# Kernel optimization log

Hardware: AMD Instinct MI355X
Metric: run time of the kernel (lower is better)

The kernel has to match this reference:

```python
import jax, jax.numpy as jnp
import numpy as np

DIM_Q, DIM_K, DIM_V, H = 256, 256, 384, 6
B, N = 8, 1024
NEG = -10.0 ** 10  # matches torch's (1 - A) * -10**10


def sparsemax(z):
    # simplex projection along last axis (Martins & Astudillo 2016)
    z = z - jnp.max(z, axis=-1, keepdims=True)  # shift-invariant, for fp stability
    z_sorted = jnp.flip(jnp.sort(z, axis=-1), axis=-1)          # descending
    k = jnp.arange(1, z.shape[-1] + 1, dtype=z.dtype)
    z_cumsum = jnp.cumsum(z_sorted, axis=-1)
    support = (1.0 + k * z_sorted) > z_cumsum
    k_z = jnp.sum(support, axis=-1, keepdims=True)              # int32 support size >= 1
    tau = (jnp.take_along_axis(z_cumsum, k_z - 1, axis=-1) - 1.0) / k_z.astype(z.dtype)
    return jnp.maximum(z - tau, 0.0)


def setup_inputs() -> dict:
    key = jax.random.key(0)
    ks = jax.random.split(key, 7)
    Q = jax.random.normal(ks[0], (B, N, DIM_Q), jnp.float32)
    V = jax.random.normal(ks[1], (B, N, DIM_K), jnp.float32)
    # binary adjacency mask with self-loops so every row has support
    A = jax.random.bernoulli(ks[2], 0.05, (B, N, N)).astype(jnp.float32)
    A = A.at[:, jnp.arange(N), jnp.arange(N)].set(1.0)
    # torch.nn.Linear default init: U(-1/sqrt(fan_in), 1/sqrt(fan_in)); weights stored pre-transposed [in, out]
    sq = 1.0 / np.sqrt(DIM_Q)
    sk = 1.0 / np.sqrt(DIM_K)
    WQ = jax.random.uniform(ks[3], (DIM_Q, DIM_V), jnp.float32, -sq, sq)
    bQ = jax.random.uniform(ks[4], (DIM_V,), jnp.float32, -sq, sq)
    WK = jax.random.uniform(ks[5], (DIM_K, DIM_V), jnp.float32, -sk, sk)
    bK = jax.random.uniform(ks[6], (DIM_V,), jnp.float32, -sk, sk)
    return {"Q": Q, "V": V, "A": A, "WQ": WQ, "bQ": bQ, "WK": WK, "bK": bK}


def reference(Q, V, A, WQ, bQ, WK, bK):
    b, n, _ = Q.shape
    d = DIM_V // H
    # project and split heads (torch split along dim=2 == reshape [b,n,H,d])
    q = (Q @ WQ + bQ).reshape(b, n, H, d).transpose(0, 2, 1, 3)   # [b,H,n,d]
    k = (V @ WK + bK).reshape(b, n, H, d).transpose(0, 2, 1, 3)   # [b,H,n,d]
    scale = 1.0 / jnp.sqrt(jnp.float32(DIM_V))
    logits = jnp.einsum('bhnd,bhmd->bhnm', q, k) * scale + (1.0 - A)[:, None] * NEG
    O = sparsemax(logits)                                          # [b,H,n,n], rows on simplex
    # torch: split(B) along dim0 then cat along dim2 -> head-major along last axis
    return O.transpose(0, 2, 1, 3).reshape(b, n, H * n)            # [b,n,H*n]
```

## Files before the change

kernel.cpp:

```cpp
#include <hip/hip_runtime.h>
#include <hip/hip_bf16.h>
#include <stdint.h>

#define DIMK 256
#define DIMV 384
#define NSEQ 1024
#define NHEAD 6
#define ZCAP 192

typedef __attribute__((ext_vector_type(8))) short short8;
typedef __attribute__((ext_vector_type(4))) float floatx4;

__device__ __forceinline__ unsigned short f2b(float f){
  unsigned int x = __float_as_uint(f);
  return (unsigned short)((x + 0x7fffu + ((x >> 16) & 1u)) >> 16);
}
__device__ __forceinline__ unsigned int pack2(float a, float b){
  return (unsigned int)f2b(a) | ((unsigned int)f2b(b) << 16);
}
__device__ __forceinline__ float blo(unsigned int u){ return __uint_as_float(u << 16); }

__global__ __launch_bounds__(256) void prep_kernel(
    const float* __restrict__ WQ, const float* __restrict__ WK,
    unsigned short* __restrict__ wqt, unsigned short* __restrict__ wkt,
    const float* __restrict__ A,
    unsigned long long* __restrict__ bm, unsigned short* __restrict__ bmp)
{
  int bid = blockIdx.x;
  if (bid < 768){
    int i = bid * 256 + threadIdx.x;
    const float* W; unsigned short* O; int idx;
    if (i < 98304){ W = WQ; O = wqt; idx = i; }
    else          { W = WK; O = wkt; idx = i - 98304; }
    int n = idx >> 8;
    int k = idx & 255;
    O[idx] = f2b(W[(size_t)k * 384 + n]);
  } else {
    int r = (bid - 768) * 4 + (threadIdx.x >> 6);
    int lane = threadIdx.x & 63;
    const float* arow = A + (size_t)r * NSEQ;
    unsigned long long myw = 0;
    #pragma unroll
    for (int c = 0; c < 16; ++c){
      unsigned long long m = __ballot(arow[c * 64 + lane] > 0.5f);
      if (lane == c) myw = m;
    }
    int own = (lane < 16) ? __popcll(myw) : 0;
    int inc = own;
    #pragma unroll
    for (int o = 1; o < 16; o <<= 1){
      int t = __shfl_up(inc, o, 16);
      if ((lane & 15) >= o) inc += t;
    }
    if (lane < 16){
      bm [(size_t)r * 16 + lane] = myw;
      bmp[(size_t)r * 16 + lane] = (unsigned short)(inc - own);
    }
  }
}

__global__ __launch_bounds__(256) void proj2_kernel(
    const float* __restrict__ Q, const float* __restrict__ V,
    const unsigned short* __restrict__ wqt, const unsigned short* __restrict__ wkt,
    const float* __restrict__ bQ, const float* __restrict__ bK,
    unsigned short* __restrict__ qhi, unsigned short* __restrict__ qlo,
    unsigned short* __restrict__ kf)
{
  __shared__ uint4 lA[512];
  __shared__ uint4 lB[864];
  int which = blockIdx.z;
  const float* X = which ? V : Q;
  const unsigned short* Wt = which ? wkt : wqt;
  const float* bias = which ? bK : bQ;

  int t = threadIdx.x;
  int lane = t & 63, wave = t >> 6;
  int wm = wave >> 1, wn = wave & 1;
  int rb = blockIdx.x * 64;
  int nb = blockIdx.y * 96;
  floatx4 acc[2][3];
  #pragma unroll
  for (int mi = 0; mi < 2; ++mi)
    #pragma unroll
    for (int ni = 0; ni < 3; ++ni) acc[mi][ni] = (floatx4){0.f, 0.f, 0.f, 0.f};

  for (int it = 0; it < 4; ++it){
    int k0 = it * 64;
    #pragma unroll
    for (int i = 0; i < 2; ++i){
      int c = t + i * 256;
      int kc = c >> 6, row = c & 63;
      const float* src = X + (size_t)(rb + row) * DIMK + k0 + kc * 8;
      float4 f0 = *(const float4*)src;
      float4 f1 = *(const float4*)(src + 4);
      uint4 w;
      w.x = pack2(f0.x, f0.y); w.y = pack2(f0.z, f0.w);
      w.z = pack2(f1.x, f1.y); w.w = pack2(f1.z, f1.w);
      lA[c] = w;
    }
    #pragma unroll
    for (int i = 0; i < 3; ++i){
      int c = t + i * 256;
      int n = c >> 3, kc = c & 7;
      uint4 v = *(const uint4*)(Wt + (size_t)(nb + n) * DIMK + k0 + kc * 8);
      lB[n * 9 + kc] = v;
    }
    __syncthreads();
    #pragma unroll
    for (int kk = 0; kk < 2; ++kk){
      int kc  = kk * 4 + (lane >> 4);
      int r16 = lane & 15;
      short8 af[2], bf[3];
      #pragma unroll
      for (int mi = 0; mi < 2; ++mi)
        af[mi] = *(const short8*)&lA[kc * 64 + wm * 32 + mi * 16 + r16];
      #pragma unroll
      for (int ni = 0; ni < 3; ++ni)
        bf[ni] = *(const short8*)&lB[(wn * 48 + ni * 16 + r16) * 9 + kc];
      #pragma unroll
      for (int mi = 0; mi < 2; ++mi)
        #pragma unroll
        for (int ni = 0; ni < 3; ++ni)
          acc[mi][ni] = __builtin_amdgcn_mfma_f32_16x16x32_bf16(af[mi], bf[ni], acc[mi][ni], 0, 0, 0);
    }
    __syncthreads();
  }
  const float scale = 0.05103103630798288f;
  int r16 = lane & 15, rq = lane >> 4;
  #pragma unroll
  for (int ni = 0; ni < 3; ++ni){
    int col = nb + wn * 48 + ni * 16 + r16;
    float bv = bias[col];
    int h = col >> 6, d = col & 63;
    #pragma unroll
    for (int mi = 0; mi < 2; ++mi){
      #pragma unroll
      for (int q = 0; q < 4; ++q){
        int row = rb + wm * 32 + mi * 16 + rq * 4 + q;
        int bb = row >> 10, n = row & 1023;
        int slice = bb * NHEAD + h;
        size_t dst = ((((size_t)slice * 2 + (d >> 5)) * 64 + (n >> 4)) * 64
                      + ((d >> 3) & 3) * 16 + (n & 15)) * 8 + (d & 7);
        float v = acc[mi][ni][q] + bv;
        if (which){
          kf[dst] = f2b(v);
        } else {
          v *= scale;
          unsigned short hi_ = f2b(v);
          qhi[dst] = hi_;
          qlo[dst] = f2b(v - blo((unsigned int)hi_));
        }
      }
    }
  }
}

__device__ __forceinline__ void red2(float& a, float& b){
  #pragma unroll
  for (int o = 1; o < 64; o <<= 1){ a += __shfl_xor(a, o); b += __shfl_xor(b, o); }
}
__device__ __forceinline__ void red4(float& a, float& b, float& c, float& d){
  #pragma unroll
  for (int o = 1; o < 64; o <<= 1){
    a += __shfl_xor(a, o); b += __shfl_xor(b, o);
    c += __shfl_xor(c, o); d += __shfl_xor(d, o);
  }
}

__global__ __launch_bounds__(512) void attn_kernel(
    const unsigned short* __restrict__ qhi, const unsigned short* __restrict__ qlo,
    const unsigned short* __restrict__ kf, const unsigned long long* __restrict__ bm,
    const unsigned short* __restrict__ bmp, float* __restrict__ out)
{
  __shared__ unsigned long long mw[16][16];
  __shared__ unsigned short    mp[16][16];
  __shared__ float             zlds[16][ZCAP + 1];

  int bid = blockIdx.x;
  int x = bid & 7;
  int u = bid >> 3;
  int h = u >> 6;
  int rb = u & 63;
  int tid = threadIdx.x;
  int lane = tid & 63, w = tid >> 6;
  int slice = x * NHEAD + h;
  int rowbase = (x << 10) + (rb << 4);

  if (tid < 256){
    int rr = tid >> 4, ww = tid & 15;
    mw[rr][ww] = bm [((size_t)(rowbase + rr)) * 16 + ww];
    mp[rr][ww] = bmp[((size_t)(rowbase + rr)) * 16 + ww];
  }

  const short8* qh8 = (const short8*)qhi;
  const short8* ql8 = (const short8*)qlo;
  const short8* kf8 = (const short8*)kf;
  size_t ab0 = (((size_t)slice * 2 + 0) * 64 + rb) * 64 + lane;
  size_t ab1 = (((size_t)slice * 2 + 1) * 64 + rb) * 64 + lane;
  short8 ah0 = qh8[ab0], al0 = ql8[ab0];
  short8 ah1 = qh8[ab1], al1 = ql8[ab1];
  __syncthreads();

  #pragma unroll
  for (int i = 0; i < 8; ++i){
    int tt = (w << 3) + i;
    short8 b0 = kf8[(((size_t)slice * 2 + 0) * 64 + tt) * 64 + lane];
    short8 b1 = kf8[(((size_t)slice * 2 + 1) * 64 + tt) * 64 + lane];
    floatx4 a = (floatx4){0.f, 0.f, 0.f, 0.f};
    a = __builtin_amdgcn_mfma_f32_16x16x32_bf16(al0, b0, a, 0, 0, 0);
    a = __builtin_amdgcn_mfma_f32_16x16x32_bf16(ah0, b0, a, 0, 0, 0);
    a = __builtin_amdgcn_mfma_f32_16x16x32_bf16(al1, b1, a, 0, 0, 0);
    a = __builtin_amdgcn_mfma_f32_16x16x32_bf16(ah1, b1, a, 0, 0, 0);
    int colb = (w << 7) + (i << 4) + (lane & 15);
    int cw = colb >> 6, cb = colb & 63;
    unsigned long long below = (1ull << cb) - 1ull;
    #pragma unroll
    for (int reg = 0; reg < 4; ++reg){
      int rowz = ((lane >> 4) << 2) + reg;
      unsigned long long word = mw[rowz][cw];
      if ((word >> cb) & 1){
        int rank = (int)mp[rowz][cw] + __popcll(word & below);
        if (rank < ZCAP) zlds[rowz][rank] = a[reg];
      }
    }
  }
  __syncthreads();

  int row0 = w * 2, row1 = w * 2 + 1;
  int M0 = (int)mp[row0][15] + __popcll(mw[row0][15]);
  int M1 = (int)mp[row1][15] + __popcll(mw[row1][15]);
  float tau0, tau1;

  if (M0 <= 64 && M1 <= 64){
    bool a0 = lane < M0, a1 = lane < M1;
    float z0 = a0 ? zlds[row0][lane] : 0.f;
    float z1 = a1 ? zlds[row1][lane] : 0.f;
    float s0 = z0, s1 = z1;
    red2(s0, s1);
    tau0 = (s0 - 1.f) / (float)M0;
    tau1 = (s1 - 1.f) / (float)M1;
    int p0 = M0, p1 = M1;
    #pragma unroll 1
    for (int it = 0; it < 32; ++it){
      bool i0 = a0 && z0 > tau0, i1 = a1 && z1 > tau1;
      int n0 = __popcll(__ballot(i0));
      int n1 = __popcll(__ballot(i1));
      s0 = i0 ? z0 : 0.f; s1 = i1 ? z1 : 0.f;
      red2(s0, s1);
      bool stable = (n0 == p0) && (n1 == p1);
      tau0 = (s0 - 1.f) / (float)n0;
      tau1 = (s1 - 1.f) / (float)n1;
      p0 = n0; p1 = n1;
      if (stable) break;
    }
  } else {
    float z0a = (lane < M0)       ? zlds[row0][lane]       : 0.f;
    float z1a = (lane < M1)       ? zlds[row1][lane]       : 0.f;
    float z0b = (64 + lane < M0)  ? zlds[row0][64 + lane]  : 0.f;
    float z1b = (64 + lane < M1)  ? zlds[row1][64 + lane]  : 0.f;
    float z0c = (128 + lane < M0) ? zlds[row0][128 + lane] : 0.f;
    float z1c = (128 + lane < M1) ? zlds[row1][128 + lane] : 0.f;
    bool a0 = lane < M0, b0_ = 64 + lane < M0, c0_ = 128 + lane < M0;
    bool a1 = lane < M1, b1_ = 64 + lane < M1, c1_ = 128 + lane < M1;
    float s0 = (a0 ? z0a : 0.f) + (b0_ ? z0b : 0.f) + (c0_ ? z0c : 0.f);
    float n0 = (a0 ? 1.f : 0.f) + (b0_ ? 1.f : 0.f) + (c0_ ? 1.f : 0.f);
    float s1 = (a1 ? z1a : 0.f) + (b1_ ? z1b : 0.f) + (c1_ ? z1c : 0.f);
    float n1 = (a1 ? 1.f : 0.f) + (b1_ ? 1.f : 0.f) + (c1_ ? 1.f : 0.f);
    red4(s0, n0, s1, n1);
    tau0 = (s0 - 1.f) / n0; tau1 = (s1 - 1.f) / n1;
    float p0 = n0, p1 = n1;
    #pragma unroll 1
    for (int it = 0; it < 32; ++it){
      bool i0a = a0 && z0a > tau0, i0b = b0_ && z0b > tau0, i0c = c0_ && z0c > tau0;
      bool i1a = a1 && z1a > tau1, i1b = b1_ && z1b > tau1, i1c = c1_ && z1c > tau1;
      s0 = (i0a ? z0a : 0.f) + (i0b ? z0b : 0.f) + (i0c ? z0c : 0.f);
      n0 = (i0a ? 1.f : 0.f) + (i0b ? 1.f : 0.f) + (i0c ? 1.f : 0.f);
      s1 = (i1a ? z1a : 0.f) + (i1b ? z1b : 0.f) + (i1c ? z1c : 0.f);
      n1 = (i1a ? 1.f : 0.f) + (i1b ? 1.f : 0.f) + (i1c ? 1.f : 0.f);
      red4(s0, n0, s1, n1);
      bool stable = (n0 == p0) && (n1 == p1);
      tau0 = (s0 - 1.f) / n0; tau1 = (s1 - 1.f) / n1;
      p0 = n0; p1 = n1;
      if (stable) break;
    }
  }

  float* o0 = out + ((size_t)(rowbase + row0) * NHEAD + h) * NSEQ;
  float* o1 = out + ((size_t)(rowbase + row1) * NHEAD + h) * NSEQ;
  int b0v = (lane & 15) << 2;
  unsigned long long pmask = (1ull << b0v) - 1ull;
  #pragma unroll
  for (int qtr = 0; qtr < 4; ++qtr){
    int cw = (qtr << 2) + (lane >> 4);
    unsigned long long w0 = mw[row0][cw], w1 = mw[row1][cw];
    int rk0 = (int)mp[row0][cw] + __popcll(w0 & pmask);
    int rk1 = (int)mp[row1][cw] + __popcll(w1 & pmask);
    float v0[4], v1[4];
    #pragma unroll
    for (int j = 0; j < 4; ++j){
      int bit0 = (int)((w0 >> (b0v + j)) & 1ull);
      int bit1 = (int)((w1 >> (b0v + j)) & 1ull);
      v0[j] = bit0 ? fmaxf(zlds[row0][rk0] - tau0, 0.f) : 0.f;
      v1[j] = bit1 ? fmaxf(zlds[row1][rk1] - tau1, 0.f) : 0.f;
      rk0 += bit0; rk1 += bit1;
    }
    ((float4*)o0)[(qtr << 6) + lane] = make_float4(v0[0], v0[1], v0[2], v0[3]);
    ((float4*)o1)[(qtr << 6) + lane] = make_float4(v1[0], v1[1], v1[2], v1[3]);
  }
}

extern "C" void kernel_launch(void* const* d_in, const int* in_sizes, int n_in,
                              void* d_out, int out_size, void* d_ws, size_t ws_size,
                              hipStream_t stream) {
  const float* Q  = (const float*)d_in[0];
  const float* V  = (const float*)d_in[1];
  const float* A  = (const float*)d_in[2];
  const float* WQ = (const float*)d_in[3];
  const float* bQ = (const float*)d_in[4];
  const float* WK = (const float*)d_in[5];
  const float* bK = (const float*)d_in[6];
  float* out = (float*)d_out;

  char* ws = (char*)d_ws;
  unsigned short*     qhi = (unsigned short*)ws;
  unsigned short*     qlo = (unsigned short*)(ws + (size_t)6291456);
  unsigned short*     kf  = (unsigned short*)(ws + (size_t)12582912);
  unsigned short*     wqt = (unsigned short*)(ws + (size_t)18874368);
  unsigned short*     wkt = (unsigned short*)(ws + (size_t)19070976);
  unsigned long long* bm  = (unsigned long long*)(ws + (size_t)19267584);
  unsigned short*     bmp = (unsigned short*)(ws + (size_t)20316160);
  (void)in_sizes; (void)n_in; (void)out_size; (void)ws_size;

  prep_kernel<<<2816, 256, 0, stream>>>(WQ, WK, wqt, wkt, A, bm, bmp);
  proj2_kernel<<<dim3(128, 4, 2), 256, 0, stream>>>(Q, V, wqt, wkt, bQ, bK, qhi, qlo, kf);
  attn_kernel<<<3072, 512, 0, stream>>>(qhi, qlo, kf, bm, bmp, out);
}
```

Measured before the change: 85.99 us.

## Fuse weight transpose, mask bitpacking and projection into one pre-kernel

Merges the weight-transpose/mask-bitmask prep kernel and the projection GEMM into a single launch. The projection blocks now read fp32 weights directly, convert them to bf16 and transpose them into shared memory, which removes the intermediate transposed-weight buffers and one kernel launch plus its dependency. It also raises wave priority around the MFMA scatter loop in the attention kernel. The cost is redundant weight conversion in every GEMM block and 2-byte scattered LDS stores that may bank-conflict.

```diff
diff --git a/kernel.cpp b/kernel.cpp
--- a/kernel.cpp
+++ b/kernel.cpp
@@ -20,23 +20,18 @@
 }
 __device__ __forceinline__ float blo(unsigned int u){ return __uint_as_float(u << 16); }
 
-__global__ __launch_bounds__(256) void prep_kernel(
+__global__ __launch_bounds__(256) void fused_pre_kernel(
+    const float* __restrict__ Q, const float* __restrict__ V,
     const float* __restrict__ WQ, const float* __restrict__ WK,
-    unsigned short* __restrict__ wqt, unsigned short* __restrict__ wkt,
+    const float* __restrict__ bQ, const float* __restrict__ bK,
     const float* __restrict__ A,
+    unsigned short* __restrict__ qhi, unsigned short* __restrict__ qlo,
+    unsigned short* __restrict__ kf,
     unsigned long long* __restrict__ bm, unsigned short* __restrict__ bmp)
 {
   int bid = blockIdx.x;
-  if (bid < 768){
-    int i = bid * 256 + threadIdx.x;
-    const float* W; unsigned short* O; int idx;
-    if (i < 98304){ W = WQ; O = wqt; idx = i; }
-    else          { W = WK; O = wkt; idx = i - 98304; }
-    int n = idx >> 8;
-    int k = idx & 255;
-    O[idx] = f2b(W[(size_t)k * 384 + n]);
-  } else {
-    int r = (bid - 768) * 4 + (threadIdx.x >> 6);
+  if (bid >= 1024){
+    int r = (bid - 1024) * 4 + (threadIdx.x >> 6);
     int lane = threadIdx.x & 63;
     const float* arow = A + (size_t)r * NSEQ;
     unsigned long long myw = 0;
@@ -56,28 +51,23 @@
       bm [(size_t)r * 16 + lane] = myw;
       bmp[(size_t)r * 16 + lane] = (unsigned short)(inc - own);
     }
-  }
-}
-
-__global__ __launch_bounds__(256) void proj2_kernel(
-    const float* __restrict__ Q, const float* __restrict__ V,
-    const unsigned short* __restrict__ wqt, const unsigned short* __restrict__ wkt,
-    const float* __restrict__ bQ, const float* __restrict__ bK,
-    unsigned short* __restrict__ qhi, unsigned short* __restrict__ qlo,
-    unsigned short* __restrict__ kf)
-{
+    return;
+  }
+
   __shared__ uint4 lA[512];
-  __shared__ uint4 lB[864];
-  int which = blockIdx.z;
+  __shared__ unsigned short lB16[96 * 72];
+  int which = bid >> 9;
+  int rem = bid & 511;
+  int bx = rem >> 2, by = rem & 3;
   const float* X = which ? V : Q;
-  const unsigned short* Wt = which ? wkt : wqt;
+  const float* W = which ? WK : WQ;
   const float* bias = which ? bK : bQ;
 
   int t = threadIdx.x;
   int lane = t & 63, wave = t >> 6;
   int wm = wave >> 1, wn = wave & 1;
-  int rb = blockIdx.x * 64;
-  int nb = blockIdx.y * 96;
+  int rb = bx * 64;
+  int nb = by * 96;
   floatx4 acc[2][3];
   #pragma unroll
   for (int mi = 0; mi < 2; ++mi)
@@ -99,11 +89,15 @@
       lA[c] = w;
     }
     #pragma unroll
-    for (int i = 0; i < 3; ++i){
+    for (int i = 0; i < 6; ++i){
       int c = t + i * 256;
-      int n = c >> 3, kc = c & 7;
-      uint4 v = *(const uint4*)(Wt + (size_t)(nb + n) * DIMK + k0 + kc * 8);
-      lB[n * 9 + kc] = v;
+      int kk2 = c / 24, f4 = c % 24;
+      float4 wv = *(const float4*)(W + (size_t)(k0 + kk2) * DIMV + nb + f4 * 4);
+      int n0 = f4 * 4;
+      lB16[(n0    ) * 72 + kk2] = f2b(wv.x);
+      lB16[(n0 + 1) * 72 + kk2] = f2b(wv.y);
+      lB16[(n0 + 2) * 72 + kk2] = f2b(wv.z);
+      lB16[(n0 + 3) * 72 + kk2] = f2b(wv.w);
     }
     __syncthreads();
     #pragma unroll
@@ -116,7 +110,7 @@
         af[mi] = *(const short8*)&lA[kc * 64 + wm * 32 + mi * 16 + r16];
       #pragma unroll
       for (int ni = 0; ni < 3; ++ni)
-        bf[ni] = *(const short8*)&lB[(wn * 48 + ni * 16 + r16) * 9 + kc];
+        bf[ni] = *(const short8*)&lB16[(wn * 48 + ni * 16 + r16) * 72 + kc * 8];
       #pragma unroll
       for (int mi = 0; mi < 2; ++mi)
         #pragma unroll
@@ -201,6 +195,7 @@
   short8 ah1 = qh8[ab1], al1 = ql8[ab1];
   __syncthreads();
 
+  __builtin_amdgcn_s_setprio(1);
   #pragma unroll
   for (int i = 0; i < 8; ++i){
     int tt = (w << 3) + i;
@@ -224,6 +219,7 @@
       }
     }
   }
+  __builtin_amdgcn_s_setprio(0);
   __syncthreads();
 
   int row0 = w * 2, row1 = w * 2 + 1;
@@ -325,13 +321,11 @@
   unsigned short*     qhi = (unsigned short*)ws;
   unsigned short*     qlo = (unsigned short*)(ws + (size_t)6291456);
   unsigned short*     kf  = (unsigned short*)(ws + (size_t)12582912);
-  unsigned short*     wqt = (unsigned short*)(ws + (size_t)18874368);
-  unsigned short*     wkt = (unsigned short*)(ws + (size_t)19070976);
   unsigned long long* bm  = (unsigned long long*)(ws + (size_t)19267584);
   unsigned short*     bmp = (unsigned short*)(ws + (size_t)20316160);
   (void)in_sizes; (void)n_in; (void)out_size; (void)ws_size;
 
-  prep_kernel<<<2816, 256, 0, stream>>>(WQ, WK, wqt, wkt, A, bm, bmp);
-  proj2_kernel<<<dim3(128, 4, 2), 256, 0, stream>>>(Q, V, wqt, wkt, bQ, bK, qhi, qlo, kf);
+  fused_pre_kernel<<<3072, 256, 0, stream>>>(Q, V, WQ, WK, bQ, bK, A,
+                                             qhi, qlo, kf, bm, bmp);
   attn_kernel<<<3072, 512, 0, stream>>>(qhi, qlo, kf, bm, bmp, out);
 }
```

Result: no change. 85.56 us (-0.5%).
